# Performance work log

Hardware: AMD Instinct MI355X
Metric: run time of the kernel (lower is better)

Reference implementation:

```python
import jax, jax.numpy as jnp
import numpy as np

K = 10
A_JAC = 0.5
B_JAC = 0.5
N_NODES = 100000
N_EDGES = 1600000
IN_CH, HID, OUT_CH = 256, 64, 32
NUM_LAYERS = 2


def setup_inputs() -> dict:
    key = jax.random.key(0)
    k1, k2, k3, k4, k5, k6 = jax.random.split(key, 6)
    x = jax.random.normal(k1, (N_NODES, IN_CH), dtype=jnp.float32)
    edge_index = jax.random.randint(k2, (2, N_EDGES), 0, N_NODES, dtype=jnp.int64)
    W1 = jax.random.normal(k3, (IN_CH, HID), dtype=jnp.float32) / np.sqrt(IN_CH)
    b1 = jnp.zeros((HID,), dtype=jnp.float32)
    coeffs = jnp.ones((NUM_LAYERS, K + 1), dtype=jnp.float32) / (K + 1)
    W2 = jax.random.normal(k4, (HID, OUT_CH), dtype=jnp.float32) / np.sqrt(HID)
    b2 = jnp.zeros((OUT_CH,), dtype=jnp.float32)
    return {"x": x, "edge_index": edge_index, "W1": W1, "b1": b1,
            "coeffs": coeffs, "W2": W2, "b2": b2}


def _build_norm(edge_index, num_nodes):
    # add self loops (as PyG add_self_loops does)
    loops = jnp.arange(num_nodes, dtype=edge_index.dtype)
    row = jnp.concatenate([edge_index[0], loops])
    col = jnp.concatenate([edge_index[1], loops])
    deg = jax.ops.segment_sum(jnp.ones_like(col, dtype=jnp.float32), col,
                              num_segments=num_nodes)
    dinv = jnp.where(deg > 0, deg ** -0.5, 0.0)
    norm = dinv[row] * dinv[col]  # [E + N]
    return row, col, norm


def _propagate(h, row, col, norm, num_nodes):
    # out[i] = sum_{e: col[e]=i} norm[e] * h[row[e]]
    return jax.ops.segment_sum(norm[:, None] * h[row], col, num_segments=num_nodes)


def _jacobi_conv(h, row, col, norm, c, num_nodes):
    a, b = A_JAC, B_JAC
    Tx0 = h
    out = c[0] * Tx0
    Tx1 = _propagate(h, row, col, norm, num_nodes)
    out = out + c[1] * Tx1
    for k in range(2, K + 1):
        n = k - 1
        A_n = (2 * n + a + b + 1) * (2 * n + a + b + 2) / (2 * (n + 1) * (n + a + b + 1))
        B_n = (a ** 2 - b ** 2) * (2 * n + a + b + 1) / (2 * (n + 1) * (n + a + b + 1) * (2 * n + a + b))
        C_n = (n + a) * (n + b) * (2 * n + a + b + 2) / ((n + 1) * (n + a + b + 1) * (2 * n + a + b))
        Tx2 = A_n * _propagate(Tx1, row, col, norm, num_nodes) + B_n * Tx1 - C_n * Tx0
        out = out + c[k] * Tx2
        Tx0, Tx1 = Tx1, Tx2
    return out


def reference(x, edge_index, W1, b1, coeffs, W2, b2):
    num_nodes = x.shape[0]
    row, col, norm = _build_norm(edge_index, num_nodes)
    h = jax.nn.relu(x @ W1 + b1)
    for l in range(NUM_LAYERS):
        h = jax.nn.relu(_jacobi_conv(h, row, col, norm, coeffs[l], num_nodes))
    return h @ W2 + b2
```

## Files before the change

### kernel.cpp

```cpp
#include <hip/hip_runtime.h>
#include <hip/hip_fp16.h>

#define NN 100000
#define NE 1600000
#define KORD 10
#define HID 64

#define NBUK ((NN + 255) / 256)
#define BCAP 8192
#define EPB  (NE / 256)
#define CSR_CAP (NE + 8 * NN)

typedef _Float16 half8v __attribute__((ext_vector_type(8)));
typedef _Float16 half4v __attribute__((ext_vector_type(4)));
typedef float float4v __attribute__((ext_vector_type(4)));

__device__ __forceinline__ float2 up2(unsigned u) {
    __half2 hh = *(__half2*)&u;
    return __half22float2(hh);
}
__device__ __forceinline__ unsigned pk2(float a, float b) {
    __half2 hh = __floats2half2_rn(a, b);
    return *(unsigned*)&hh;
}

__global__ __launch_bounds__(512) void k_zero(int* __restrict__ gcnt,
                                              int* __restrict__ dhist,
                                              int* __restrict__ palloc) {
    int t = threadIdx.x;
    if (t < NBUK) gcnt[t] = 0;
    if (t < 64) dhist[t] = 0;
    if (t == 511) *palloc = 0;
}

__global__ __launch_bounds__(1024) void k_binA(const int* __restrict__ ei,
                                               int* __restrict__ gcnt,
                                               unsigned* __restrict__ staged) {
    __shared__ int lh[NBUK];
    __shared__ int lcur[NBUK];
    int t = threadIdx.x;
    int ebeg = blockIdx.x * EPB;
    int eend = min(ebeg + EPB, NE);
    for (int i = t; i < NBUK; i += 1024) lh[i] = 0;
    __syncthreads();
    for (int e = ebeg + t; e < eend; e += 1024)
        atomicAdd(&lh[ei[NE + e] >> 8], 1);
    __syncthreads();
    for (int i = t; i < NBUK; i += 1024)
        lcur[i] = lh[i] ? atomicAdd(&gcnt[i], lh[i]) : 0;
    __syncthreads();
    for (int e = ebeg + t; e < eend; e += 1024) {
        int r = ei[e], c = ei[NE + e];
        int bkt = c >> 8;
        int slot = atomicAdd(&lcur[bkt], 1);
        if (slot < BCAP)
            staged[(size_t)bkt * BCAP + slot] = ((unsigned)(c & 255) << 24) | (unsigned)r;
    }
}

__global__ __launch_bounds__(512) void k_binB(const unsigned* __restrict__ staged,
                                              const int* __restrict__ gcnt,
                                              int* __restrict__ palloc,
                                              int* __restrict__ cnt,
                                              float* __restrict__ dinv,
                                              int* __restrict__ csr,
                                              int2* __restrict__ seg) {
    __shared__ unsigned lrec[BCAP];
    __shared__ int lcnt[256], lcur[256], ltmp[256];
    __shared__ int lbase;
    int b = blockIdx.x, t = threadIdx.x;
    int count = min(gcnt[b], BCAP);
    if (t < 256) lcnt[t] = 0;
    __syncthreads();
    for (int i = t; i < count; i += 512) {
        unsigned rec = staged[(size_t)b * BCAP + i];
        lrec[i] = rec;
        atomicAdd(&lcnt[rec >> 24], 1);
    }
    __syncthreads();
    int v = 0, plen = 0;
    if (t < 256) { v = lcnt[t]; plen = (v + 7) & ~7; ltmp[t] = plen; }
    __syncthreads();
    int x = plen;
    for (int off = 1; off < 256; off <<= 1) {
        int y = (t < 256 && t >= off) ? ltmp[t - off] : 0;
        __syncthreads();
        if (t < 256) { x += y; ltmp[t] = x; }
        __syncthreads();
    }
    if (t == 255) lbase = atomicAdd(palloc, x);
    __syncthreads();
    int start = 0;
    if (t < 256) {
        start = lbase + x - plen;
        lcur[t] = start;
        int node = b * 256 + t;
        if (node < NN) {
            cnt[node] = v;
            dinv[node] = rsqrtf((float)(v + 1));
            seg[node] = make_int2(start, plen >> 3);
            for (int i = v; i < plen; ++i) csr[start + i] = NN;
        }
    }
    __syncthreads();
    for (int i = t; i < count; i += 512) {
        unsigned rec = lrec[i];
        int pos = atomicAdd(&lcur[rec >> 24], 1);
        csr[pos] = (int)(rec & 0xFFFFFFu);
    }
}

__global__ __launch_bounds__(256) void k_dhist(const int* __restrict__ cnt,
                                               int* __restrict__ dhist) {
    __shared__ int lh[64];
    int t = threadIdx.x;
    if (t < 64) lh[t] = 0;
    __syncthreads();
    int i = blockIdx.x * 256 + t;
    if (i < NN) atomicAdd(&lh[min(cnt[i], 63)], 1);
    __syncthreads();
    if (t < 64 && lh[t]) atomicAdd(&dhist[t], lh[t]);
}

__global__ void k_dscan(int* __restrict__ dhist) {
    __shared__ int tmp[64];
    int t = threadIdx.x;
    int v = dhist[t];
    tmp[t] = v;
    __syncthreads();
    int x = v;
    for (int off = 1; off < 64; off <<= 1) {
        int y = (t >= off) ? tmp[t - off] : 0;
        __syncthreads();
        x += y;
        tmp[t] = x;
        __syncthreads();
    }
    dhist[t] = x - v;
}

__global__ __launch_bounds__(256) void k_dperm(const int* __restrict__ cnt,
                                               int* __restrict__ dhist,
                                               int* __restrict__ perm) {
    __shared__ int lh[64], lb[64];
    int t = threadIdx.x;
    if (t < 64) lh[t] = 0;
    __syncthreads();
    int i = blockIdx.x * 256 + t;
    int b = 0, my = 0;
    if (i < NN) { b = min(cnt[i], 63); my = atomicAdd(&lh[b], 1); }
    __syncthreads();
    if (t < 64) lb[t] = lh[t] ? atomicAdd(&dhist[t], lh[t]) : 0;
    __syncthreads();
    if (i < NN) perm[lb[b] + my] = i;
}

__global__ __launch_bounds__(256) void k_zrow(__half* __restrict__ a, __half* __restrict__ b,
                                              __half* __restrict__ c, __half* __restrict__ d) {
    int t = threadIdx.x;
    __half z = __float2half(0.f);
    size_t base = (size_t)NN * HID;
    if (t < 64)       a[base + t] = z;
    else if (t < 128) b[base + (t - 64)] = z;
    else if (t < 192) c[base + (t - 128)] = z;
    else              d[base + (t - 192)] = z;
}

__global__ __launch_bounds__(256) void k_prepw1(const float* __restrict__ W1,
                                                _Float16* __restrict__ W1T) {
    int f = blockIdx.x * 256 + threadIdx.x;
    int n = f >> 8, k = f & 255;
    W1T[f] = (_Float16)W1[k * 64 + n];
}

#define G1K 128
#define G1S 136
__global__ __launch_bounds__(256) void k_gemm1(const float* __restrict__ x,
                                               const _Float16* __restrict__ W1T,
                                               const float* __restrict__ b1,
                                               const float* __restrict__ dinv,
                                               __half* __restrict__ h) {
    __shared__ _Float16 A_lds[64 * G1S];
    __shared__ _Float16 B_lds[64 * G1S];
    int t = threadIdx.x;
    int wave = t >> 6, lane = t & 63;
    int quad = lane >> 4, m16 = lane & 15;
    int row0 = blockIdx.x * 64;

    float4v acc[4];
#pragma unroll
    for (int n4 = 0; n4 < 4; ++n4) acc[n4] = (float4v){0.f, 0.f, 0.f, 0.f};

    for (int c = 0; c < 2; ++c) {
        int k0 = c * G1K;
#pragma unroll
        for (int i = 0; i < 8; ++i) {
            int f = i * 256 + t;
            int r = f >> 5, c4 = f & 31;
            int grow = row0 + r;
            float4 v = (grow < NN) ? *(const float4*)&x[(size_t)grow * 256 + k0 + c4 * 4]
                                   : make_float4(0.f, 0.f, 0.f, 0.f);
            half4v hv = {(_Float16)v.x, (_Float16)v.y, (_Float16)v.z, (_Float16)v.w};
            *(half4v*)&A_lds[r * G1S + c4 * 4] = hv;
        }
#pragma unroll
        for (int i = 0; i < 4; ++i) {
            int f = i * 256 + t;
            int n = f >> 4, k8 = f & 15;
            *(half8v*)&B_lds[n * G1S + k8 * 8] =
                *(const half8v*)&W1T[n * 256 + k0 + k8 * 8];
        }
        __syncthreads();

#pragma unroll
        for (int s = 0; s < 4; ++s) {
            half8v af = *(const half8v*)&A_lds[(wave * 16 + m16) * G1S + s * 32 + quad * 8];
#pragma unroll
            for (int n4 = 0; n4 < 4; ++n4) {
                half8v bf = *(const half8v*)&B_lds[(n4 * 16 + m16) * G1S + s * 32 + quad * 8];
                acc[n4] = __builtin_amdgcn_mfma_f32_16x16x32_f16(af, bf, acc[n4], 0, 0, 0);
            }
        }
        __syncthreads();
    }

    float bv[4];
#pragma unroll
    for (int n4 = 0; n4 < 4; ++n4) bv[n4] = b1[n4 * 16 + m16];
#pragma unroll
    for (int r = 0; r < 4; ++r) {
        int grow = row0 + wave * 16 + quad * 4 + r;
        if (grow >= NN) continue;
        float dv = dinv[grow];
#pragma unroll
        for (int n4 = 0; n4 < 4; ++n4) {
            float v = dv * fmaxf(acc[n4][r] + bv[n4], 0.f);
            h[(size_t)grow * 64 + n4 * 16 + m16] = __float2half(v);
        }
    }
}

#define ACC8(u) { float2 f0 = up2((u).x), f1 = up2((u).y), f2 = up2((u).z), f3 = up2((u).w); \
    p[0] += f0.x; p[1] += f0.y; p[2] += f1.x; p[3] += f1.y; \
    p[4] += f2.x; p[5] += f2.y; p[6] += f3.x; p[7] += f3.y; }

__global__ __launch_bounds__(256) void k_prop(const int2* __restrict__ seg,
                                              const int* __restrict__ csr,
                                              const int* __restrict__ perm,
                                              const __half* __restrict__ src,
                                              const __half* __restrict__ t0,
                                              const float* __restrict__ dinv,
                                              __half* __restrict__ dst,
                                              __half* __restrict__ acc,
                                              __half* __restrict__ hout,
                                              float An, float Bn, float Cn,
                                              const float* __restrict__ coeffs,
                                              int cbase, int kidx, int init,
                                              int finalize, int unscale) {
    int slot = ((blockIdx.x * 256 + threadIdx.x) >> 6) * 8 + ((threadIdx.x & 63) >> 3);
    int ch8 = (threadIdx.x & 7) * 8;
    bool valid = slot < NN;
    int node = valid ? perm[slot] : 0;
    int2 sg = valid ? seg[node] : make_int2(0, 0);
    const int4* cp = (const int4*)(csr + sg.x);
    int iters = sg.y;

    float p[8];
#pragma unroll
    for (int i = 0; i < 8; ++i) p[i] = 0.f;

    for (int it = 0; it < iters; ++it) {
        int4 ia = cp[it * 2];
        int4 ib = cp[it * 2 + 1];
        uint4 u0 = *(const uint4*)&src[(size_t)ia.x * HID + ch8];
        uint4 u1 = *(const uint4*)&src[(size_t)ia.y * HID + ch8];
        uint4 u2 = *(const uint4*)&src[(size_t)ia.z * HID + ch8];
        uint4 u3 = *(const uint4*)&src[(size_t)ia.w * HID + ch8];
        uint4 u4 = *(const uint4*)&src[(size_t)ib.x * HID + ch8];
        uint4 u5 = *(const uint4*)&src[(size_t)ib.y * HID + ch8];
        uint4 u6 = *(const uint4*)&src[(size_t)ib.z * HID + ch8];
        uint4 u7 = *(const uint4*)&src[(size_t)ib.w * HID + ch8];
        ACC8(u0); ACC8(u1); ACC8(u2); ACC8(u3);
        ACC8(u4); ACC8(u5); ACC8(u6); ACC8(u7);
    }

    if (!valid) return;
    size_t idx = (size_t)node * HID + ch8;
    float dv = dinv[node];
    float dv2 = dv * dv;

    uint4 sr = *(const uint4*)&src[idx];
    float2 s01 = up2(sr.x), s23 = up2(sr.y), s45 = up2(sr.z), s67 = up2(sr.w);
    float sv[8] = {s01.x, s01.y, s23.x, s23.y, s45.x, s45.y, s67.x, s67.y};

    uint4 tr = *(const uint4*)&t0[idx];
    float2 t01 = up2(tr.x), t23 = up2(tr.y), t45 = up2(tr.z), t67 = up2(tr.w);
    float tv[8] = {t01.x, t01.y, t23.x, t23.y, t45.x, t45.y, t67.x, t67.y};

    float v[8];
#pragma unroll
    for (int i = 0; i < 8; ++i)
        v[i] = An * dv2 * (p[i] + sv[i]) + Bn * sv[i] - Cn * tv[i];

    if (!finalize) {
        uint4 o;
        o.x = pk2(v[0], v[1]); o.y = pk2(v[2], v[3]);
        o.z = pk2(v[4], v[5]); o.w = pk2(v[6], v[7]);
        *(uint4*)&dst[idx] = o;
    }

    float ck = coeffs[cbase + kidx];
    float av[8];
    if (init) {
        float c0 = coeffs[cbase];
#pragma unroll
        for (int i = 0; i < 8; ++i) av[i] = c0 * sv[i];
    } else {
        uint4 ar = *(const uint4*)&acc[idx];
        float2 a01 = up2(ar.x), a23 = up2(ar.y), a45 = up2(ar.z), a67 = up2(ar.w);
        av[0] = a01.x; av[1] = a01.y; av[2] = a23.x; av[3] = a23.y;
        av[4] = a45.x; av[5] = a45.y; av[6] = a67.x; av[7] = a67.y;
    }
#pragma unroll
    for (int i = 0; i < 8; ++i) av[i] += ck * v[i];

    uint4 o;
    if (finalize) {
        float s = unscale ? (1.0f / dv) : 1.0f;
        o.x = pk2(s * fmaxf(av[0], 0.f), s * fmaxf(av[1], 0.f));
        o.y = pk2(s * fmaxf(av[2], 0.f), s * fmaxf(av[3], 0.f));
        o.z = pk2(s * fmaxf(av[4], 0.f), s * fmaxf(av[5], 0.f));
        o.w = pk2(s * fmaxf(av[6], 0.f), s * fmaxf(av[7], 0.f));
        *(uint4*)&hout[idx] = o;
    } else {
        o.x = pk2(av[0], av[1]); o.y = pk2(av[2], av[3]);
        o.z = pk2(av[4], av[5]); o.w = pk2(av[6], av[7]);
        *(uint4*)&acc[idx] = o;
    }
}

__global__ __launch_bounds__(256) void k_gemm2(const __half* __restrict__ h,
                                               const float* __restrict__ W2,
                                               const float* __restrict__ b2,
                                               float* __restrict__ out) {
    __shared__ float W2s[64 * 32];
    __shared__ float b2s[32];
    int t = threadIdx.x;
    for (int i = t * 4; i < 64 * 32; i += 256 * 4)
        *(float4*)&W2s[i] = *(const float4*)&W2[i];
    if (t < 32) b2s[t] = b2[t];
    __syncthreads();

    int gid = blockIdx.x * 256 + t;
    int row = gid >> 3;
    int c4 = (t & 7) * 4;
    if (row >= NN) return;
    const __half* hr = h + (size_t)row * 64;
    float4 acc = *(const float4*)&b2s[c4];
#pragma unroll
    for (int k8 = 0; k8 < 8; ++k8) {
        uint4 raw = *(const uint4*)&hr[k8 * 8];
        float2 a01 = up2(raw.x), a23 = up2(raw.y), a45 = up2(raw.z), a67 = up2(raw.w);
        float a[8] = {a01.x, a01.y, a23.x, a23.y, a45.x, a45.y, a67.x, a67.y};
#pragma unroll
        for (int j = 0; j < 8; ++j) {
            float4 w = *(const float4*)&W2s[(k8 * 8 + j) * 32 + c4];
            acc.x += a[j] * w.x;
            acc.y += a[j] * w.y;
            acc.z += a[j] * w.z;
            acc.w += a[j] * w.w;
        }
    }
    *(float4*)&out[(size_t)row * 32 + c4] = acc;
}

extern "C" void kernel_launch(void* const* d_in, const int* in_sizes, int n_in,
                              void* d_out, int out_size, void* d_ws, size_t ws_size,
                              hipStream_t stream) {
    const float* x      = (const float*)d_in[0];
    const int*   ei     = (const int*)d_in[1];
    const float* W1     = (const float*)d_in[2];
    const float* b1     = (const float*)d_in[3];
    const float* coeffs = (const float*)d_in[4];
    const float* W2     = (const float*)d_in[5];
    const float* b2     = (const float*)d_in[6];
    float* out = (float*)d_out;

    char* ws = (char*)d_ws;
    size_t off = 0;
    auto alloc = [&](size_t bytes) { void* p = ws + off; off += (bytes + 255) & ~(size_t)255; return p; };
    int*      cnt    = (int*)alloc(NN * 4);
    float*    dinv   = (float*)alloc(NN * 4);
    int*      csr    = (int*)alloc((size_t)CSR_CAP * 4);
    int2*     seg    = (int2*)alloc((size_t)NN * 8);
    int*      dhist  = (int*)alloc(64 * 4);
    int*      perm   = (int*)alloc(NN * 4);
    int*      gcnt   = (int*)alloc(NBUK * 4);
    int*      palloc = (int*)alloc(4);
    unsigned* staged = (unsigned*)alloc((size_t)NBUK * BCAP * 4);
    _Float16* W1T    = (_Float16*)alloc(256 * 64 * 2);
    __half*   h16    = (__half*)alloc((size_t)(NN + 1) * HID * 2);
    __half*   bufA   = (__half*)alloc((size_t)(NN + 1) * HID * 2);
    __half*   bufB   = (__half*)alloc((size_t)(NN + 1) * HID * 2);
    __half*   bufC   = (__half*)alloc((size_t)(NN + 1) * HID * 2);
    __half*   accb   = (__half*)alloc((size_t)NN * HID * 2);

    const int BN = (NN + 255) / 256;
    const int BP = (NN + 31) / 32;

    k_zero<<<1, 512, 0, stream>>>(gcnt, dhist, palloc);
    k_binA<<<256, 1024, 0, stream>>>(ei, gcnt, staged);
    k_binB<<<NBUK, 512, 0, stream>>>(staged, gcnt, palloc, cnt, dinv, csr, seg);

    k_dhist<<<BN, 256, 0, stream>>>(cnt, dhist);
    k_dscan<<<1, 64, 0, stream>>>(dhist);
    k_dperm<<<BN, 256, 0, stream>>>(cnt, dhist, perm);
    k_zrow<<<1, 256, 0, stream>>>(h16, bufA, bufB, bufC);

    k_prepw1<<<64, 256, 0, stream>>>(W1, W1T);
    k_gemm1<<<(NN + 63) / 64, 256, 0, stream>>>(x, W1T, b1, dinv, h16);

    __half* rot[4] = {h16, bufA, bufB, bufC};

    for (int l = 0; l < 2; ++l) {
        int cbase = l * (KORD + 1);
        k_prop<<<BP, 256, 0, stream>>>(seg, csr, perm, rot[0], rot[0], dinv,
                                       rot[1], accb, h16, 1.0f, 0.0f, 0.0f,
                                       coeffs, cbase, 1, 1, 0, 0);
        for (int k = 2; k <= KORD; ++k) {
            __half* dst = rot[k & 3];
            const __half* s1 = rot[(k - 1) & 3];
            const __half* s0 = rot[(k - 2) & 3];
            double n = k - 1, a = 0.5, b = 0.5;
            double An = (2*n + a + b + 1) * (2*n + a + b + 2) / (2 * (n + 1) * (n + a + b + 1));
            double Bn = (a*a - b*b) * (2*n + a + b + 1) / (2 * (n + 1) * (n + a + b + 1) * (2*n + a + b));
            double Cn = (n + a) * (n + b) * (2*n + a + b + 2) / ((n + 1) * (n + a + b + 1) * (2*n + a + b));
            k_prop<<<BP, 256, 0, stream>>>(seg, csr, perm, s1, s0, dinv,
                                           dst, accb, h16, (float)An, (float)Bn, (float)Cn,
                                           coeffs, cbase, k, 0,
                                           (k == KORD) ? 1 : 0, l);
        }
    }

    k_gemm2<<<(NN * 8 + 255) / 256, 256, 0, stream>>>(h16, W2, b2, out);
}
```

Baseline: 995.0 us.

## Split feature buffers into four 16-channel slices and propagate per slice

Re-lays out all hidden feature buffers as four planar slices of 16 channels per node. The propagation kernel now runs one grid section per slice, so each gather touches a smaller working set that fits better in cache. Two threads cover a node's 16 channels instead of eight threads covering 64. Streaming loads and stores (CSR indices, t0, acc, dst) are marked nontemporal so they do not evict the gathered source rows. The cost is that CSR indices and node metadata are read four times per propagation.

Result: slower. 2.128 ms (+113.9%).

```diff
diff --git a/kernel.cpp b/kernel.cpp
--- a/kernel.cpp
+++ b/kernel.cpp
@@ -11,9 +11,15 @@
 #define EPB  (NE / 256)
 #define CSR_CAP (NE + 8 * NN)
 
+#define NSL 4
+#define SROW (NN + 1)
+#define NBPS ((NN + 127) / 128)
+
 typedef _Float16 half8v __attribute__((ext_vector_type(8)));
 typedef _Float16 half4v __attribute__((ext_vector_type(4)));
 typedef float float4v __attribute__((ext_vector_type(4)));
+typedef unsigned uint4v __attribute__((ext_vector_type(4)));
+typedef int int4v __attribute__((ext_vector_type(4)));
 
 __device__ __forceinline__ float2 up2(unsigned u) {
     __half2 hh = *(__half2*)&u;
@@ -158,12 +164,9 @@
 __global__ __launch_bounds__(256) void k_zrow(__half* __restrict__ a, __half* __restrict__ b,
                                               __half* __restrict__ c, __half* __restrict__ d) {
     int t = threadIdx.x;
-    __half z = __float2half(0.f);
-    size_t base = (size_t)NN * HID;
-    if (t < 64)       a[base + t] = z;
-    else if (t < 128) b[base + (t - 64)] = z;
-    else if (t < 192) c[base + (t - 128)] = z;
-    else              d[base + (t - 192)] = z;
+    __half* bufs[4] = {a, b, c, d};
+    int bi = t >> 6, s = (t >> 4) & 3, ch = t & 15;
+    bufs[bi][((size_t)s * SROW + NN) * 16 + ch] = __float2half(0.f);
 }
 
 __global__ __launch_bounds__(256) void k_prepw1(const float* __restrict__ W1,
@@ -235,7 +238,7 @@
 #pragma unroll
         for (int n4 = 0; n4 < 4; ++n4) {
             float v = dv * fmaxf(acc[n4][r] + bv[n4], 0.f);
-            h[(size_t)grow * 64 + n4 * 16 + m16] = __float2half(v);
+            h[((size_t)n4 * SROW + grow) * 16 + m16] = __float2half(v);
         }
     }
 }
@@ -257,43 +260,47 @@
                                               const float* __restrict__ coeffs,
                                               int cbase, int kidx, int init,
                                               int finalize, int unscale) {
-    int slot = ((blockIdx.x * 256 + threadIdx.x) >> 6) * 8 + ((threadIdx.x & 63) >> 3);
-    int ch8 = (threadIdx.x & 7) * 8;
+    int sl  = blockIdx.x / NBPS;
+    int blk = blockIdx.x - sl * NBPS;
+    int t = threadIdx.x;
+    int slot = blk * 128 + (t >> 6) * 32 + ((t & 63) >> 1);
+    int ch8 = (t & 1) * 8;
     bool valid = slot < NN;
     int node = valid ? perm[slot] : 0;
     int2 sg = valid ? seg[node] : make_int2(0, 0);
-    const int4* cp = (const int4*)(csr + sg.x);
+    const int4v* cp = (const int4v*)(csr + sg.x);
     int iters = sg.y;
+    const __half* sb = src + (size_t)sl * SROW * 16;
 
     float p[8];
 #pragma unroll
     for (int i = 0; i < 8; ++i) p[i] = 0.f;
 
     for (int it = 0; it < iters; ++it) {
-        int4 ia = cp[it * 2];
-        int4 ib = cp[it * 2 + 1];
-        uint4 u0 = *(const uint4*)&src[(size_t)ia.x * HID + ch8];
-        uint4 u1 = *(const uint4*)&src[(size_t)ia.y * HID + ch8];
-        uint4 u2 = *(const uint4*)&src[(size_t)ia.z * HID + ch8];
-        uint4 u3 = *(const uint4*)&src[(size_t)ia.w * HID + ch8];
-        uint4 u4 = *(const uint4*)&src[(size_t)ib.x * HID + ch8];
-        uint4 u5 = *(const uint4*)&src[(size_t)ib.y * HID + ch8];
-        uint4 u6 = *(const uint4*)&src[(size_t)ib.z * HID + ch8];
-        uint4 u7 = *(const uint4*)&src[(size_t)ib.w * HID + ch8];
+        int4v ia = __builtin_nontemporal_load(&cp[it * 2]);
+        int4v ib = __builtin_nontemporal_load(&cp[it * 2 + 1]);
+        uint4v u0 = *(const uint4v*)&sb[ia.x * 16 + ch8];
+        uint4v u1 = *(const uint4v*)&sb[ia.y * 16 + ch8];
+        uint4v u2 = *(const uint4v*)&sb[ia.z * 16 + ch8];
+        uint4v u3 = *(const uint4v*)&sb[ia.w * 16 + ch8];
+        uint4v u4 = *(const uint4v*)&sb[ib.x * 16 + ch8];
+        uint4v u5 = *(const uint4v*)&sb[ib.y * 16 + ch8];
+        uint4v u6 = *(const uint4v*)&sb[ib.z * 16 + ch8];
+        uint4v u7 = *(const uint4v*)&sb[ib.w * 16 + ch8];
         ACC8(u0); ACC8(u1); ACC8(u2); ACC8(u3);
         ACC8(u4); ACC8(u5); ACC8(u6); ACC8(u7);
     }
 
     if (!valid) return;
-    size_t idx = (size_t)node * HID + ch8;
+    size_t idx = ((size_t)sl * SROW + node) * 16 + ch8;
     float dv = dinv[node];
     float dv2 = dv * dv;
 
-    uint4 sr = *(const uint4*)&src[idx];
+    uint4v sr = *(const uint4v*)&src[idx];
     float2 s01 = up2(sr.x), s23 = up2(sr.y), s45 = up2(sr.z), s67 = up2(sr.w);
     float sv[8] = {s01.x, s01.y, s23.x, s23.y, s45.x, s45.y, s67.x, s67.y};
 
-    uint4 tr = *(const uint4*)&t0[idx];
+    uint4v tr = __builtin_nontemporal_load((const uint4v*)&t0[idx]);
     float2 t01 = up2(tr.x), t23 = up2(tr.y), t45 = up2(tr.z), t67 = up2(tr.w);
     float tv[8] = {t01.x, t01.y, t23.x, t23.y, t45.x, t45.y, t67.x, t67.y};
 
@@ -303,10 +310,10 @@
         v[i] = An * dv2 * (p[i] + sv[i]) + Bn * sv[i] - Cn * tv[i];
 
     if (!finalize) {
-        uint4 o;
+        uint4v o;
         o.x = pk2(v[0], v[1]); o.y = pk2(v[2], v[3]);
         o.z = pk2(v[4], v[5]); o.w = pk2(v[6], v[7]);
-        *(uint4*)&dst[idx] = o;
+        __builtin_nontemporal_store(o, (uint4v*)&dst[idx]);
     }
 
     float ck = coeffs[cbase + kidx];
@@ -316,7 +323,7 @@
 #pragma unroll
         for (int i = 0; i < 8; ++i) av[i] = c0 * sv[i];
     } else {
-        uint4 ar = *(const uint4*)&acc[idx];
+        uint4v ar = __builtin_nontemporal_load((const uint4v*)&acc[idx]);
         float2 a01 = up2(ar.x), a23 = up2(ar.y), a45 = up2(ar.z), a67 = up2(ar.w);
         av[0] = a01.x; av[1] = a01.y; av[2] = a23.x; av[3] = a23.y;
         av[4] = a45.x; av[5] = a45.y; av[6] = a67.x; av[7] = a67.y;
@@ -324,18 +331,18 @@
 #pragma unroll
     for (int i = 0; i < 8; ++i) av[i] += ck * v[i];
 
-    uint4 o;
+    uint4v o;
     if (finalize) {
         float s = unscale ? (1.0f / dv) : 1.0f;
         o.x = pk2(s * fmaxf(av[0], 0.f), s * fmaxf(av[1], 0.f));
         o.y = pk2(s * fmaxf(av[2], 0.f), s * fmaxf(av[3], 0.f));
         o.z = pk2(s * fmaxf(av[4], 0.f), s * fmaxf(av[5], 0.f));
         o.w = pk2(s * fmaxf(av[6], 0.f), s * fmaxf(av[7], 0.f));
-        *(uint4*)&hout[idx] = o;
+        __builtin_nontemporal_store(o, (uint4v*)&hout[idx]);
     } else {
         o.x = pk2(av[0], av[1]); o.y = pk2(av[2], av[3]);
         o.z = pk2(av[4], av[5]); o.w = pk2(av[6], av[7]);
-        *(uint4*)&acc[idx] = o;
+        __builtin_nontemporal_store(o, (uint4v*)&acc[idx]);
     }
 }
 
@@ -355,20 +362,23 @@
     int row = gid >> 3;
     int c4 = (t & 7) * 4;
     if (row >= NN) return;
-    const __half* hr = h + (size_t)row * 64;
     float4 acc = *(const float4*)&b2s[c4];
 #pragma unroll
-    for (int k8 = 0; k8 < 8; ++k8) {
-        uint4 raw = *(const uint4*)&hr[k8 * 8];
-        float2 a01 = up2(raw.x), a23 = up2(raw.y), a45 = up2(raw.z), a67 = up2(raw.w);
-        float a[8] = {a01.x, a01.y, a23.x, a23.y, a45.x, a45.y, a67.x, a67.y};
-#pragma unroll
-        for (int j = 0; j < 8; ++j) {
-            float4 w = *(const float4*)&W2s[(k8 * 8 + j) * 32 + c4];
-            acc.x += a[j] * w.x;
-            acc.y += a[j] * w.y;
-            acc.z += a[j] * w.z;
-            acc.w += a[j] * w.w;
+    for (int s = 0; s < 4; ++s) {
+        const __half* hr = h + ((size_t)s * SROW + row) * 16;
+#pragma unroll
+        for (int p8 = 0; p8 < 2; ++p8) {
+            uint4 raw = *(const uint4*)&hr[p8 * 8];
+            float2 a01 = up2(raw.x), a23 = up2(raw.y), a45 = up2(raw.z), a67 = up2(raw.w);
+            float a[8] = {a01.x, a01.y, a23.x, a23.y, a45.x, a45.y, a67.x, a67.y};
+#pragma unroll
+            for (int j = 0; j < 8; ++j) {
+                float4 w = *(const float4*)&W2s[(s * 16 + p8 * 8 + j) * 32 + c4];
+                acc.x += a[j] * w.x;
+                acc.y += a[j] * w.y;
+                acc.z += a[j] * w.z;
+                acc.w += a[j] * w.w;
+            }
         }
     }
     *(float4*)&out[(size_t)row * 32 + c4] = acc;
@@ -399,14 +409,14 @@
     int*      palloc = (int*)alloc(4);
     unsigned* staged = (unsigned*)alloc((size_t)NBUK * BCAP * 4);
     _Float16* W1T    = (_Float16*)alloc(256 * 64 * 2);
-    __half*   h16    = (__half*)alloc((size_t)(NN + 1) * HID * 2);
-    __half*   bufA   = (__half*)alloc((size_t)(NN + 1) * HID * 2);
-    __half*   bufB   = (__half*)alloc((size_t)(NN + 1) * HID * 2);
-    __half*   bufC   = (__half*)alloc((size_t)(NN + 1) * HID * 2);
-    __half*   accb   = (__half*)alloc((size_t)NN * HID * 2);
+    __half*   h16    = (__half*)alloc((size_t)NSL * SROW * 16 * 2);
+    __half*   bufA   = (__half*)alloc((size_t)NSL * SROW * 16 * 2);
+    __half*   bufB   = (__half*)alloc((size_t)NSL * SROW * 16 * 2);
+    __half*   bufC   = (__half*)alloc((size_t)NSL * SROW * 16 * 2);
+    __half*   accb   = (__half*)alloc((size_t)NSL * SROW * 16 * 2);
 
     const int BN = (NN + 255) / 256;
-    const int BP = (NN + 31) / 32;
+    const int BPP = NBPS * NSL;
 
     k_zero<<<1, 512, 0, stream>>>(gcnt, dhist, palloc);
     k_binA<<<256, 1024, 0, stream>>>(ei, gcnt, staged);
@@ -424,9 +434,9 @@
 
     for (int l = 0; l < 2; ++l) {
         int cbase = l * (KORD + 1);
-        k_prop<<<BP, 256, 0, stream>>>(seg, csr, perm, rot[0], rot[0], dinv,
-                                       rot[1], accb, h16, 1.0f, 0.0f, 0.0f,
-                                       coeffs, cbase, 1, 1, 0, 0);
+        k_prop<<<BPP, 256, 0, stream>>>(seg, csr, perm, rot[0], rot[0], dinv,
+                                        rot[1], accb, h16, 1.0f, 0.0f, 0.0f,
+                                        coeffs, cbase, 1, 1, 0, 0);
         for (int k = 2; k <= KORD; ++k) {
             __half* dst = rot[k & 3];
             const __half* s1 = rot[(k - 1) & 3];
@@ -435,10 +445,10 @@
             double An = (2*n + a + b + 1) * (2*n + a + b + 2) / (2 * (n + 1) * (n + a + b + 1));
             double Bn = (a*a - b*b) * (2*n + a + b + 1) / (2 * (n + 1) * (n + a + b + 1) * (2*n + a + b));
             double Cn = (n + a) * (n + b) * (2*n + a + b + 2) / ((n + 1) * (n + a + b + 1) * (2*n + a + b));
-            k_prop<<<BP, 256, 0, stream>>>(seg, csr, perm, s1, s0, dinv,
-                                           dst, accb, h16, (float)An, (float)Bn, (float)Cn,
-                                           coeffs, cbase, k, 0,
-                                           (k == KORD) ? 1 : 0, l);
+            k_prop<<<BPP, 256, 0, stream>>>(seg, csr, perm, s1, s0, dinv,
+                                            dst, accb, h16, (float)An, (float)Bn, (float)Cn,
+                                            coeffs, cbase, k, 0,
+                                            (k == KORD) ? 1 : 0, l);
         }
     }
 
```
